# Performance work log

Measured on AMD Instinct MI355X. Metric: run time of the kernel, lower is better.

Reference implementation:

```python
import jax, jax.numpy as jnp
import numpy as np

B, T, C, H = 4, 2048, 1024, 16
HD = C // H
INIT_SCALE = 0.25

def setup_inputs() -> dict:
    key = jax.random.key(0)
    k1, k2, k3 = jax.random.split(key, 3)
    x = jax.random.normal(k1, (B, T, C), dtype=jnp.float32)
    W_attn = jax.random.normal(k2, (3 * C, C), dtype=jnp.float32) * INIT_SCALE  # torch Linear weight [out,in]
    b_attn = jnp.zeros((3 * C,), dtype=jnp.float32)
    W_proj = jax.random.normal(k3, (C, C), dtype=jnp.float32) * INIT_SCALE
    b_proj = jnp.zeros((C,), dtype=jnp.float32)
    return {"x": x, "W_attn": W_attn, "b_attn": b_attn, "W_proj": W_proj, "b_proj": b_proj}

def reference(x, W_attn, b_attn, W_proj, b_proj):
    # fused QKV projection: [B,T,3C]
    qkv = x @ W_attn.T + b_attn
    q, k, v = jnp.split(qkv, 3, axis=-1)  # each [B,T,C]
    # [B,H,T,HD]
    q = q.reshape(B, T, H, HD).transpose(0, 2, 1, 3)
    k = k.reshape(B, T, H, HD).transpose(0, 2, 1, 3)
    v = v.reshape(B, T, H, HD).transpose(0, 2, 1, 3)
    scale = 1.0 / jnp.sqrt(jnp.asarray(HD, dtype=q.dtype))
    attn = jnp.einsum('bhqd,bhkd->bhqk', q, k) * scale  # [B,H,T,T]
    attn = jax.nn.softmax(attn, axis=-1)
    out = jnp.einsum('bhqk,bhkd->bhqd', attn, v)  # [B,H,T,HD]
    out = out.transpose(0, 2, 1, 3).reshape(B, T, C)
    return out @ W_proj.T + b_proj
```

## Files before the change

kernel.cpp:

```cpp
#include <hip/hip_runtime.h>
#include <hip/hip_bf16.h>

#define BB 4
#define TT 2048
#define CC 1024
#define HH 16
#define HD 64

typedef _Float16 half8 __attribute__((ext_vector_type(8)));
typedef _Float16 half4 __attribute__((ext_vector_type(4)));
typedef _Float16 half2_t __attribute__((ext_vector_type(2)));
typedef __fp16 fp16x2 __attribute__((ext_vector_type(2)));
typedef float floatx4 __attribute__((ext_vector_type(4)));

__device__ __forceinline__ void async_cp16(const void* g, void* l) {
    __builtin_amdgcn_global_load_lds(
        (const __attribute__((address_space(1))) unsigned int*)g,
        (__attribute__((address_space(3))) unsigned int*)l,
        16, 0, 0);
}

__device__ __forceinline__ float exp2_raw(float x) {
    return __builtin_amdgcn_exp2f(x);
}

__device__ __forceinline__ half4 pack4(float p0, float p1, float p2, float p3) {
    fp16x2 lo = __builtin_amdgcn_cvt_pkrtz(p0, p1);
    fp16x2 hi = __builtin_amdgcn_cvt_pkrtz(p2, p3);
    return __builtin_bit_cast(half4, __builtin_shufflevector(lo, hi, 0, 1, 2, 3));
}

__device__ __forceinline__ float max16(const floatx4 s[4]) {
    float a0 = fmaxf(fmaxf(s[0][0], s[0][1]), s[0][2]);
    float a1 = fmaxf(fmaxf(s[0][3], s[1][0]), s[1][1]);
    float a2 = fmaxf(fmaxf(s[1][2], s[1][3]), s[2][0]);
    float a3 = fmaxf(fmaxf(s[2][1], s[2][2]), s[2][3]);
    float a4 = fmaxf(fmaxf(s[3][0], s[3][1]), s[3][2]);
    float b0 = fmaxf(fmaxf(a0, a1), a2);
    float b1 = fmaxf(fmaxf(a3, a4), s[3][3]);
    return fmaxf(b0, b1);
}

__global__ void cvt_f32_f16(const float* __restrict__ src, _Float16* __restrict__ dst, int n) {
    int i = (blockIdx.x * blockDim.x + threadIdx.x) * 8;
    if (i < n) {
        float4 v0 = *(const float4*)(src + i);
        float4 v1 = *(const float4*)(src + i + 4);
        half8 h;
        h[0] = (_Float16)v0.x; h[1] = (_Float16)v0.y; h[2] = (_Float16)v0.z; h[3] = (_Float16)v0.w;
        h[4] = (_Float16)v1.x; h[5] = (_Float16)v1.y; h[6] = (_Float16)v1.z; h[7] = (_Float16)v1.w;
        *(half8*)(dst + i) = h;
    }
}

template <int EPI>
__global__ __launch_bounds__(256) void hgemm_nt(
    const _Float16* __restrict__ A, const _Float16* __restrict__ Bw,
    const float* __restrict__ bias,
    _Float16* __restrict__ q_out, _Float16* __restrict__ k_out, _Float16* __restrict__ v_out,
    float* __restrict__ c_out,
    int M, int N, int K)
{
    __shared__ __attribute__((aligned(16))) _Float16 As[2 * 128 * 32];
    __shared__ __attribute__((aligned(16))) _Float16 Bs[2 * 128 * 32];

    const int tid  = threadIdx.x;
    const int lane = tid & 63;
    const int wave = tid >> 6;
    const int quad = lane >> 4;
    const int lc   = lane & 15;
    const int wr   = wave >> 1, wc = wave & 1;
    const size_t bm = (size_t)blockIdx.y * 128;
    const size_t bn = (size_t)blockIdx.x * 128;

    const int r0 = tid >> 2;
    const int ck = (tid & 3) * 8;

    const _Float16* Ap = A + (bm + r0) * (size_t)K + ck;
    const _Float16* Bp = Bw + (bn + r0) * (size_t)K + ck;
    _Float16* lA = As + tid * 8;
    _Float16* lB = Bs + tid * 8;
    const size_t rstep = (size_t)64 * K;

    floatx4 acc[4][4] = {};

    for (int kk = 0; kk < K; kk += 64) {
        __syncthreads();
        async_cp16(Ap + kk, lA);
        async_cp16(Ap + kk + rstep, lA + 2048);
        async_cp16(Ap + kk + 32, lA + 4096);
        async_cp16(Ap + kk + 32 + rstep, lA + 4096 + 2048);
        async_cp16(Bp + kk, lB);
        async_cp16(Bp + kk + rstep, lB + 2048);
        async_cp16(Bp + kk + 32, lB + 4096);
        async_cp16(Bp + kk + 32 + rstep, lB + 4096 + 2048);
        __syncthreads();

#pragma unroll
        for (int h = 0; h < 2; h++) {
            half8 af[4], bf[4];
#pragma unroll
            for (int mt = 0; mt < 4; mt++)
                af[mt] = *(const half8*)(As + h * 4096 + (wr * 64 + mt * 16 + lc) * 32 + quad * 8);
#pragma unroll
            for (int nt = 0; nt < 4; nt++)
                bf[nt] = *(const half8*)(Bs + h * 4096 + (wc * 64 + nt * 16 + lc) * 32 + quad * 8);
#pragma unroll
            for (int mt = 0; mt < 4; mt++)
#pragma unroll
                for (int nt = 0; nt < 4; nt++)
                    acc[mt][nt] = __builtin_amdgcn_mfma_f32_16x16x32_f16(af[mt], bf[nt], acc[mt][nt], 0, 0, 0);
        }
    }

#pragma unroll
    for (int mt = 0; mt < 4; mt++) {
        int mbase = (int)bm + wr * 64 + mt * 16 + quad * 4;
#pragma unroll
        for (int nt = 0; nt < 4; nt++) {
            int n = (int)bn + wc * 64 + nt * 16 + lc;
            float bv = bias[n];
#pragma unroll
            for (int r = 0; r < 4; r++) {
                float v = acc[mt][nt][r] + bv;
                int mm = mbase + r;
                if (EPI == 0) {
                    int seg = n >> 10;
                    int cm  = n & 1023;
                    int h = cm >> 6, d = cm & 63;
                    int bb = mm >> 11, t = mm & 2047;
                    size_t dst = (((size_t)(bb * HH + h)) * TT + t) * HD + d;
                    if (seg == 0)      q_out[dst] = (_Float16)(v * 0.18033688f);
                    else if (seg == 1) k_out[dst] = (_Float16)v;
                    else               v_out[dst] = (_Float16)v;
                } else {
                    c_out[(size_t)mm * N + n] = v;
                }
            }
        }
    }
}

__global__ __launch_bounds__(512) void attn_flash(
    const _Float16* __restrict__ Qp, const _Float16* __restrict__ Kp,
    const _Float16* __restrict__ Vp, _Float16* __restrict__ Op)
{
    __shared__ __attribute__((aligned(16))) _Float16 Ks[64][72];
    __shared__ __attribute__((aligned(16))) _Float16 Vt[64][76];

    const int bh   = blockIdx.x;
    const int qt   = blockIdx.y;
    const int tid  = threadIdx.x;
    const int lane = tid & 63;
    const int wave = tid >> 6;
    const int quad = lane >> 4;
    const int lc   = lane & 15;

    const size_t hb = (size_t)bh * TT * HD;
    const _Float16* Kh = Kp + hb;
    const _Float16* Vh = Vp + hb;

    const int q0row = qt * 256 + wave * 32 + lc;
    const int q1row = q0row + 16;
    half8 bq00 = *(const half8*)(Qp + hb + (size_t)q0row * HD + quad * 8);
    half8 bq01 = *(const half8*)(Qp + hb + (size_t)q0row * HD + 32 + quad * 8);
    half8 bq10 = *(const half8*)(Qp + hb + (size_t)q1row * HD + quad * 8);
    half8 bq11 = *(const half8*)(Qp + hb + (size_t)q1row * HD + 32 + quad * 8);

    floatx4 o0[4] = {}, o1[4] = {};
    float m0 = -1e30f, l0 = 0.f, m1 = -1e30f, l1 = 0.f;

    const int sk  = tid >> 3;
    const int sc0 = (tid & 7) * 8;
    const int vkp = tid >> 4;
    const int vd4 = (tid & 15) * 4;

    const _Float16* Kg  = Kh + (size_t)sk * HD + sc0;
    const _Float16* Vg0 = Vh + (size_t)(2 * vkp) * HD + vd4;
    const _Float16* Vg1 = Vg0 + HD;

    for (int kt = 0; kt < TT; kt += 64) {
        const size_t koff = (size_t)kt * HD;
        half8 kv  = *(const half8*)(Kg + koff);
        half4 va0 = *(const half4*)(Vg0 + koff);
        half4 vb0 = *(const half4*)(Vg1 + koff);
        __syncthreads();
        *(half8*)&Ks[sk][sc0] = kv;
#pragma unroll
        for (int j = 0; j < 4; j++) {
            half2_t w; w[0] = va0[j]; w[1] = vb0[j];
            *(half2_t*)&Vt[vd4 + j][2 * vkp] = w;
        }
        __syncthreads();

        floatx4 s0[4], s1[4];
        const floatx4 zf = {0.f, 0.f, 0.f, 0.f};
        __builtin_amdgcn_s_setprio(1);
#pragma unroll
        for (int m = 0; m < 4; m++) {
            half8 a0 = *(const half8*)&Ks[m * 16 + lc][quad * 8];
            half8 a1 = *(const half8*)&Ks[m * 16 + lc][32 + quad * 8];
            s0[m] = __builtin_amdgcn_mfma_f32_16x16x32_f16(a0, bq00, zf, 0, 0, 0);
            s0[m] = __builtin_amdgcn_mfma_f32_16x16x32_f16(a1, bq01, s0[m], 0, 0, 0);
            s1[m] = __builtin_amdgcn_mfma_f32_16x16x32_f16(a0, bq10, zf, 0, 0, 0);
            s1[m] = __builtin_amdgcn_mfma_f32_16x16x32_f16(a1, bq11, s1[m], 0, 0, 0);
        }
        __builtin_amdgcn_s_setprio(0);

        half4 pf0[4], pf1[4];
        {
            float mx = max16(s0);
            mx = fmaxf(mx, __shfl_xor(mx, 16));
            mx = fmaxf(mx, __shfl_xor(mx, 32));
            const bool noresc = __all(mx <= m0 + 8.0f);
            const float mnew = noresc ? m0 : fmaxf(m0, mx);
            float rs = 0.f;
#pragma unroll
            for (int m = 0; m < 4; m++) {
                float p0 = exp2_raw(s0[m][0] - mnew);
                float p1 = exp2_raw(s0[m][1] - mnew);
                float p2 = exp2_raw(s0[m][2] - mnew);
                float p3 = exp2_raw(s0[m][3] - mnew);
                rs += (p0 + p1) + (p2 + p3);
                pf0[m] = pack4(p0, p1, p2, p3);
            }
            rs += __shfl_xor(rs, 16);
            rs += __shfl_xor(rs, 32);
            if (!noresc) {
                float al = exp2_raw(m0 - mnew);
                m0 = mnew;
                l0 *= al;
#pragma unroll
                for (int dt = 0; dt < 4; dt++) o0[dt] *= al;
            }
            l0 += rs;
        }
        {
            float mx = max16(s1);
            mx = fmaxf(mx, __shfl_xor(mx, 16));
            mx = fmaxf(mx, __shfl_xor(mx, 32));
            const bool noresc = __all(mx <= m1 + 8.0f);
            const float mnew = noresc ? m1 : fmaxf(m1, mx);
            float rs = 0.f;
#pragma unroll
            for (int m = 0; m < 4; m++) {
                float p0 = exp2_raw(s1[m][0] - mnew);
                float p1 = exp2_raw(s1[m][1] - mnew);
                float p2 = exp2_raw(s1[m][2] - mnew);
                float p3 = exp2_raw(s1[m][3] - mnew);
                rs += (p0 + p1) + (p2 + p3);
                pf1[m] = pack4(p0, p1, p2, p3);
            }
            rs += __shfl_xor(rs, 16);
            rs += __shfl_xor(rs, 32);
            if (!noresc) {
                float al = exp2_raw(m1 - mnew);
                m1 = mnew;
                l1 *= al;
#pragma unroll
                for (int dt = 0; dt < 4; dt++) o1[dt] *= al;
            }
            l1 += rs;
        }

        __builtin_amdgcn_s_setprio(1);
#pragma unroll
        for (int dt = 0; dt < 4; dt++) {
            const _Float16* vr = &Vt[dt * 16 + lc][quad * 4];
#pragma unroll
            for (int m = 0; m < 4; m++) {
                half4 va = *(const half4*)(vr + m * 16);
                o0[dt] = __builtin_amdgcn_mfma_f32_16x16x16f16(va, pf0[m], o0[dt], 0, 0, 0);
                o1[dt] = __builtin_amdgcn_mfma_f32_16x16x16f16(va, pf1[m], o1[dt], 0, 0, 0);
            }
        }
        __builtin_amdgcn_s_setprio(0);
    }

    const int b = bh >> 4, h = bh & 15;
    {
        float inv = __builtin_amdgcn_rcpf(l0);
        size_t base = ((size_t)(b * TT + q0row)) * CC + h * HD;
#pragma unroll
        for (int dt = 0; dt < 4; dt++) {
            half4 hv;
#pragma unroll
            for (int r = 0; r < 4; r++) hv[r] = (_Float16)(o0[dt][r] * inv);
            *(half4*)(Op + base + dt * 16 + quad * 4) = hv;
        }
    }
    {
        float inv = __builtin_amdgcn_rcpf(l1);
        size_t base = ((size_t)(b * TT + q1row)) * CC + h * HD;
#pragma unroll
        for (int dt = 0; dt < 4; dt++) {
            half4 hv;
#pragma unroll
            for (int r = 0; r < 4; r++) hv[r] = (_Float16)(o1[dt][r] * inv);
            *(half4*)(Op + base + dt * 16 + quad * 4) = hv;
        }
    }
}

extern "C" void kernel_launch(void* const* d_in, const int* in_sizes, int n_in,
                              void* d_out, int out_size, void* d_ws, size_t ws_size,
                              hipStream_t stream) {
    const float* x      = (const float*)d_in[0];
    const float* W_attn = (const float*)d_in[1];
    const float* b_attn = (const float*)d_in[2];
    const float* W_proj = (const float*)d_in[3];
    const float* b_proj = (const float*)d_in[4];
    float* out = (float*)d_out;

    const size_t SZ_XH  = (size_t)BB * TT * CC * 2;
    const size_t SZ_WA  = (size_t)3 * CC * CC * 2;
    const size_t SZ_WP  = (size_t)CC * CC * 2;
    const size_t SZ_QKV = (size_t)BB * HH * TT * HD * 2;
    size_t off = 0;
    _Float16* xh  = (_Float16*)((char*)d_ws + off); off += SZ_XH;
    _Float16* wah = (_Float16*)((char*)d_ws + off); off += SZ_WA;
    _Float16* wph = (_Float16*)((char*)d_ws + off); off += SZ_WP;
    _Float16* Qh  = (_Float16*)((char*)d_ws + off); off += SZ_QKV;
    _Float16* Kh  = (_Float16*)((char*)d_ws + off); off += SZ_QKV;
    _Float16* Vh  = (_Float16*)((char*)d_ws + off); off += SZ_QKV;
    _Float16* Ah  = (_Float16*)((char*)d_ws + off); off += SZ_XH;
    if (ws_size < off) return;

    const int NX  = BB * TT * CC;
    const int NWA = 3 * CC * CC;
    const int NWP = CC * CC;
    cvt_f32_f16<<<NX / 8 / 256, 256, 0, stream>>>(x, xh, NX);
    cvt_f32_f16<<<NWA / 8 / 256, 256, 0, stream>>>(W_attn, wah, NWA);
    cvt_f32_f16<<<NWP / 8 / 256, 256, 0, stream>>>(W_proj, wph, NWP);

    hgemm_nt<0><<<dim3(3 * CC / 128, BB * TT / 128), 256, 0, stream>>>(
        xh, wah, b_attn, Qh, Kh, Vh, nullptr, BB * TT, 3 * CC, CC);

    attn_flash<<<dim3(BB * HH, TT / 256), 512, 0, stream>>>(Qh, Kh, Vh, Ah);

    hgemm_nt<1><<<dim3(CC / 128, BB * TT / 128), 256, 0, stream>>>(
        Ah, wph, b_proj, nullptr, nullptr, nullptr, out, BB * TT, CC, CC);
}
```

Before: 291.9 us.

## Switch flash attention to 32x32x16 MFMA with swizzled LDS and permlane P repack

Rewrites the attention inner loop to use 32x32x16 f16 MFMAs instead of 16x16 tiles. Each wave now owns 32 query rows with a single running max and sum, so the softmax reductions need fewer shuffles. The K and V tiles in LDS move from padded rows to an XOR-swizzled layout to avoid bank conflicts. The probability tile is repacked into the MFMA B-operand layout with permlane32_swap instead of going through LDS. The aim is fewer MFMA issues, less softmax bookkeeping and cheaper LDS reads, at the cost of more complex fragment layout logic that has to be exactly right.

```diff
diff --git a/kernel.cpp b/kernel.cpp
--- a/kernel.cpp
+++ b/kernel.cpp
@@ -12,6 +12,9 @@
 typedef _Float16 half2_t __attribute__((ext_vector_type(2)));
 typedef __fp16 fp16x2 __attribute__((ext_vector_type(2)));
 typedef float floatx4 __attribute__((ext_vector_type(4)));
+typedef float floatx16 __attribute__((ext_vector_type(16)));
+typedef int intx2 __attribute__((ext_vector_type(2)));
+typedef int intx4 __attribute__((ext_vector_type(4)));
 
 __device__ __forceinline__ void async_cp16(const void* g, void* l) {
     __builtin_amdgcn_global_load_lds(
@@ -24,21 +27,33 @@
     return __builtin_amdgcn_exp2f(x);
 }
 
+__device__ __forceinline__ int pkh(float a, float b) {
+    fp16x2 v = __builtin_amdgcn_cvt_pkrtz(a, b);
+    return __builtin_bit_cast(int, v);
+}
+
 __device__ __forceinline__ half4 pack4(float p0, float p1, float p2, float p3) {
     fp16x2 lo = __builtin_amdgcn_cvt_pkrtz(p0, p1);
     fp16x2 hi = __builtin_amdgcn_cvt_pkrtz(p2, p3);
     return __builtin_bit_cast(half4, __builtin_shufflevector(lo, hi, 0, 1, 2, 3));
 }
 
-__device__ __forceinline__ float max16(const floatx4 s[4]) {
-    float a0 = fmaxf(fmaxf(s[0][0], s[0][1]), s[0][2]);
-    float a1 = fmaxf(fmaxf(s[0][3], s[1][0]), s[1][1]);
-    float a2 = fmaxf(fmaxf(s[1][2], s[1][3]), s[2][0]);
-    float a3 = fmaxf(fmaxf(s[2][1], s[2][2]), s[2][3]);
-    float a4 = fmaxf(fmaxf(s[3][0], s[3][1]), s[3][2]);
+__device__ __forceinline__ float maxv16(floatx16 s) {
+    float a0 = fmaxf(fmaxf(s[0], s[1]), s[2]);
+    float a1 = fmaxf(fmaxf(s[3], s[4]), s[5]);
+    float a2 = fmaxf(fmaxf(s[6], s[7]), s[8]);
+    float a3 = fmaxf(fmaxf(s[9], s[10]), s[11]);
+    float a4 = fmaxf(fmaxf(s[12], s[13]), s[14]);
     float b0 = fmaxf(fmaxf(a0, a1), a2);
-    float b1 = fmaxf(fmaxf(a3, a4), s[3][3]);
+    float b1 = fmaxf(fmaxf(a3, a4), s[15]);
     return fmaxf(b0, b1);
+}
+
+__device__ __forceinline__ half8 assembleF(int a, int b, int c, int d) {
+    intx2 s1 = __builtin_amdgcn_permlane32_swap(a, c, false, false);
+    intx2 s2 = __builtin_amdgcn_permlane32_swap(b, d, false, false);
+    intx4 w = {s1[0], s2[0], s1[1], s2[1]};
+    return __builtin_bit_cast(half8, w);
 }
 
 __global__ void cvt_f32_f16(const float* __restrict__ src, _Float16* __restrict__ dst, int n) {
@@ -145,38 +160,37 @@
     const _Float16* __restrict__ Qp, const _Float16* __restrict__ Kp,
     const _Float16* __restrict__ Vp, _Float16* __restrict__ Op)
 {
-    __shared__ __attribute__((aligned(16))) _Float16 Ks[64][72];
-    __shared__ __attribute__((aligned(16))) _Float16 Vt[64][76];
+    __shared__ __attribute__((aligned(16))) _Float16 Ks[64 * 64];
+    __shared__ __attribute__((aligned(16))) _Float16 Vt[64 * 64];
 
     const int bh   = blockIdx.x;
     const int qt   = blockIdx.y;
     const int tid  = threadIdx.x;
     const int lane = tid & 63;
     const int wave = tid >> 6;
-    const int quad = lane >> 4;
-    const int lc   = lane & 15;
+    const int ql   = lane & 31;
+    const int hi   = lane >> 5;
 
     const size_t hb = (size_t)bh * TT * HD;
-    const _Float16* Kh = Kp + hb;
-    const _Float16* Vh = Vp + hb;
-
-    const int q0row = qt * 256 + wave * 32 + lc;
-    const int q1row = q0row + 16;
-    half8 bq00 = *(const half8*)(Qp + hb + (size_t)q0row * HD + quad * 8);
-    half8 bq01 = *(const half8*)(Qp + hb + (size_t)q0row * HD + 32 + quad * 8);
-    half8 bq10 = *(const half8*)(Qp + hb + (size_t)q1row * HD + quad * 8);
-    half8 bq11 = *(const half8*)(Qp + hb + (size_t)q1row * HD + 32 + quad * 8);
-
-    floatx4 o0[4] = {}, o1[4] = {};
-    float m0 = -1e30f, l0 = 0.f, m1 = -1e30f, l1 = 0.f;
-
-    const int sk  = tid >> 3;
-    const int sc0 = (tid & 7) * 8;
+
+    const int qrow = qt * 256 + wave * 32 + ql;
+    half8 bq[4];
+#pragma unroll
+    for (int c = 0; c < 4; c++)
+        bq[c] = *(const half8*)(Qp + hb + (size_t)qrow * HD + c * 16 + hi * 8);
+
+    floatx16 o0 = (floatx16)0.0f, o1 = (floatx16)0.0f;
+    float mrun = -1e30f, lrun = 0.f;
+
+    const int sk = tid >> 3;
+    const int sj = tid & 7;
+    const int sg = sj ^ (sk & 7);
+    const _Float16* Kg = Kp + hb + (size_t)sk * HD + sg * 8;
+    _Float16* KsW = Ks + tid * 8;
+
     const int vkp = tid >> 4;
     const int vd4 = (tid & 15) * 4;
-
-    const _Float16* Kg  = Kh + (size_t)sk * HD + sc0;
-    const _Float16* Vg0 = Vh + (size_t)(2 * vkp) * HD + vd4;
+    const _Float16* Vg0 = Vp + hb + (size_t)(2 * vkp) * HD + vd4;
     const _Float16* Vg1 = Vg0 + HD;
 
     for (int kt = 0; kt < TT; kt += 64) {
@@ -185,120 +199,89 @@
         half4 va0 = *(const half4*)(Vg0 + koff);
         half4 vb0 = *(const half4*)(Vg1 + koff);
         __syncthreads();
-        *(half8*)&Ks[sk][sc0] = kv;
+        *(half8*)KsW = kv;
 #pragma unroll
         for (int j = 0; j < 4; j++) {
+            int row = vd4 + j;
+            int boff = (row * 128 + vkp * 4) ^ ((row & 7) << 4);
             half2_t w; w[0] = va0[j]; w[1] = vb0[j];
-            *(half2_t*)&Vt[vd4 + j][2 * vkp] = w;
+            *(half2_t*)((char*)Vt + boff) = w;
         }
         __syncthreads();
 
-        floatx4 s0[4], s1[4];
-        const floatx4 zf = {0.f, 0.f, 0.f, 0.f};
+        floatx16 s0 = (floatx16)0.0f, s1 = (floatx16)0.0f;
         __builtin_amdgcn_s_setprio(1);
 #pragma unroll
-        for (int m = 0; m < 4; m++) {
-            half8 a0 = *(const half8*)&Ks[m * 16 + lc][quad * 8];
-            half8 a1 = *(const half8*)&Ks[m * 16 + lc][32 + quad * 8];
-            s0[m] = __builtin_amdgcn_mfma_f32_16x16x32_f16(a0, bq00, zf, 0, 0, 0);
-            s0[m] = __builtin_amdgcn_mfma_f32_16x16x32_f16(a1, bq01, s0[m], 0, 0, 0);
-            s1[m] = __builtin_amdgcn_mfma_f32_16x16x32_f16(a0, bq10, zf, 0, 0, 0);
-            s1[m] = __builtin_amdgcn_mfma_f32_16x16x32_f16(a1, bq11, s1[m], 0, 0, 0);
+        for (int c = 0; c < 4; c++) {
+            int offk = (ql * 128 + c * 32 + hi * 16) ^ ((ql & 7) << 4);
+            half8 a0 = *(const half8*)((const char*)Ks + offk);
+            half8 a1 = *(const half8*)((const char*)Ks + offk + 4096);
+            s0 = __builtin_amdgcn_mfma_f32_32x32x16_f16(a0, bq[c], s0, 0, 0, 0);
+            s1 = __builtin_amdgcn_mfma_f32_32x32x16_f16(a1, bq[c], s1, 0, 0, 0);
         }
         __builtin_amdgcn_s_setprio(0);
 
-        half4 pf0[4], pf1[4];
-        {
-            float mx = max16(s0);
-            mx = fmaxf(mx, __shfl_xor(mx, 16));
-            mx = fmaxf(mx, __shfl_xor(mx, 32));
-            const bool noresc = __all(mx <= m0 + 8.0f);
-            const float mnew = noresc ? m0 : fmaxf(m0, mx);
-            float rs = 0.f;
-#pragma unroll
-            for (int m = 0; m < 4; m++) {
-                float p0 = exp2_raw(s0[m][0] - mnew);
-                float p1 = exp2_raw(s0[m][1] - mnew);
-                float p2 = exp2_raw(s0[m][2] - mnew);
-                float p3 = exp2_raw(s0[m][3] - mnew);
-                rs += (p0 + p1) + (p2 + p3);
-                pf0[m] = pack4(p0, p1, p2, p3);
-            }
-            rs += __shfl_xor(rs, 16);
-            rs += __shfl_xor(rs, 32);
-            if (!noresc) {
-                float al = exp2_raw(m0 - mnew);
-                m0 = mnew;
-                l0 *= al;
-#pragma unroll
-                for (int dt = 0; dt < 4; dt++) o0[dt] *= al;
-            }
-            l0 += rs;
-        }
-        {
-            float mx = max16(s1);
-            mx = fmaxf(mx, __shfl_xor(mx, 16));
-            mx = fmaxf(mx, __shfl_xor(mx, 32));
-            const bool noresc = __all(mx <= m1 + 8.0f);
-            const float mnew = noresc ? m1 : fmaxf(m1, mx);
-            float rs = 0.f;
-#pragma unroll
-            for (int m = 0; m < 4; m++) {
-                float p0 = exp2_raw(s1[m][0] - mnew);
-                float p1 = exp2_raw(s1[m][1] - mnew);
-                float p2 = exp2_raw(s1[m][2] - mnew);
-                float p3 = exp2_raw(s1[m][3] - mnew);
-                rs += (p0 + p1) + (p2 + p3);
-                pf1[m] = pack4(p0, p1, p2, p3);
-            }
-            rs += __shfl_xor(rs, 16);
-            rs += __shfl_xor(rs, 32);
-            if (!noresc) {
-                float al = exp2_raw(m1 - mnew);
-                m1 = mnew;
-                l1 *= al;
-#pragma unroll
-                for (int dt = 0; dt < 4; dt++) o1[dt] *= al;
-            }
-            l1 += rs;
-        }
+        float mx = fmaxf(maxv16(s0), maxv16(s1));
+        mx = fmaxf(mx, __shfl_xor(mx, 32));
+        const bool noresc = __all(mx <= mrun + 8.0f);
+        const float mnew = noresc ? mrun : fmaxf(mrun, mx);
+        float rs = 0.f;
+        int d[16];
+#pragma unroll
+        for (int i = 0; i < 8; i++) {
+            float e0 = exp2_raw(s0[2 * i] - mnew);
+            float e1 = exp2_raw(s0[2 * i + 1] - mnew);
+            rs += e0 + e1;
+            d[i] = pkh(e0, e1);
+        }
+#pragma unroll
+        for (int i = 0; i < 8; i++) {
+            float e0 = exp2_raw(s1[2 * i] - mnew);
+            float e1 = exp2_raw(s1[2 * i + 1] - mnew);
+            rs += e0 + e1;
+            d[8 + i] = pkh(e0, e1);
+        }
+        rs += __shfl_xor(rs, 32);
+        if (!noresc) {
+            float al = exp2_raw(mrun - mnew);
+            mrun = mnew;
+            lrun *= al;
+            o0 *= al;
+            o1 *= al;
+        }
+        lrun += rs;
+
+        half8 F[4];
+        F[0] = assembleF(d[0], d[1], d[2], d[3]);
+        F[1] = assembleF(d[4], d[5], d[6], d[7]);
+        F[2] = assembleF(d[8], d[9], d[10], d[11]);
+        F[3] = assembleF(d[12], d[13], d[14], d[15]);
 
         __builtin_amdgcn_s_setprio(1);
 #pragma unroll
-        for (int dt = 0; dt < 4; dt++) {
-            const _Float16* vr = &Vt[dt * 16 + lc][quad * 4];
-#pragma unroll
-            for (int m = 0; m < 4; m++) {
-                half4 va = *(const half4*)(vr + m * 16);
-                o0[dt] = __builtin_amdgcn_mfma_f32_16x16x16f16(va, pf0[m], o0[dt], 0, 0, 0);
-                o1[dt] = __builtin_amdgcn_mfma_f32_16x16x16f16(va, pf1[m], o1[dt], 0, 0, 0);
-            }
+        for (int kb = 0; kb < 4; kb++) {
+            int offv = (ql * 128 + kb * 32 + hi * 16) ^ ((ql & 7) << 4);
+            half8 v0 = *(const half8*)((const char*)Vt + offv);
+            half8 v1 = *(const half8*)((const char*)Vt + offv + 4096);
+            o0 = __builtin_amdgcn_mfma_f32_32x32x16_f16(v0, F[kb], o0, 0, 0, 0);
+            o1 = __builtin_amdgcn_mfma_f32_32x32x16_f16(v1, F[kb], o1, 0, 0, 0);
         }
         __builtin_amdgcn_s_setprio(0);
     }
 
+    const float inv = __builtin_amdgcn_rcpf(lrun);
     const int b = bh >> 4, h = bh & 15;
-    {
-        float inv = __builtin_amdgcn_rcpf(l0);
-        size_t base = ((size_t)(b * TT + q0row)) * CC + h * HD;
-#pragma unroll
-        for (int dt = 0; dt < 4; dt++) {
-            half4 hv;
-#pragma unroll
-            for (int r = 0; r < 4; r++) hv[r] = (_Float16)(o0[dt][r] * inv);
-            *(half4*)(Op + base + dt * 16 + quad * 4) = hv;
-        }
-    }
-    {
-        float inv = __builtin_amdgcn_rcpf(l1);
-        size_t base = ((size_t)(b * TT + q1row)) * CC + h * HD;
-#pragma unroll
-        for (int dt = 0; dt < 4; dt++) {
-            half4 hv;
-#pragma unroll
-            for (int r = 0; r < 4; r++) hv[r] = (_Float16)(o1[dt][r] * inv);
-            *(half4*)(Op + base + dt * 16 + quad * 4) = hv;
-        }
+    size_t base = ((size_t)(b * TT + qrow)) * CC + h * HD;
+#pragma unroll
+    for (int rr = 0; rr < 4; rr++) {
+        half4 hv0, hv1;
+#pragma unroll
+        for (int t = 0; t < 4; t++) {
+            hv0[t] = (_Float16)(o0[rr * 4 + t] * inv);
+            hv1[t] = (_Float16)(o1[rr * 4 + t] * inv);
+        }
+        *(half4*)(Op + base + 8 * rr + 4 * hi) = hv0;
+        *(half4*)(Op + base + 32 + 8 * rr + 4 * hi) = hv1;
     }
 }
 
```

Result: no change. 288.5 us (-1.2%).
